# Kernel tuning notes

Measured on AMD Instinct MI355X. Metric: run time of the kernel, lower is better.

Reference implementation:

```python
import math
import jax, jax.numpy as jnp
import numpy as np

NUM_BUCKETS = 32
MAX_DISTANCE = 128
B, T, E, H, D = 2, 2048, 1024, 16, 64
INIT_SCALE = 0.1


def _relative_position_bucket(rel, num_buckets=NUM_BUCKETS, max_distance=MAX_DISTANCE):
    # T5-style bucketing; rel is int [T, T]
    nb = num_buckets // 2
    buckets = (rel > 0).astype(jnp.int32) * nb
    rel_abs = jnp.abs(rel)
    max_exact = nb // 2
    is_small = rel_abs < max_exact
    # guard log(0); those positions are selected by is_small anyway
    val_large = max_exact + (
        jnp.log(jnp.maximum(rel_abs, 1).astype(jnp.float32) / max_exact)
        / math.log(max_distance / max_exact) * (nb - max_exact)
    ).astype(jnp.int32)
    val_large = jnp.minimum(val_large, nb - 1)
    return buckets + jnp.where(is_small, rel_abs, val_large)


def setup_inputs() -> dict:
    key = jax.random.key(0)
    ks = jax.random.split(key, 6)
    x = jax.random.normal(ks[0], (B, T, E), dtype=jnp.float32)
    # nn.Linear weights are [out_features, in_features], init normal(std=0.1)
    Wq = jax.random.normal(ks[1], (H * D, E), dtype=jnp.float32) * INIT_SCALE
    Wk = jax.random.normal(ks[2], (H * D, E), dtype=jnp.float32) * INIT_SCALE
    Wv = jax.random.normal(ks[3], (H * D, E), dtype=jnp.float32) * INIT_SCALE
    Wo = jax.random.normal(ks[4], (E, H * D), dtype=jnp.float32) * INIT_SCALE
    # nn.Embedding default init: standard normal
    rel_emb = jax.random.normal(ks[5], (NUM_BUCKETS, H), dtype=jnp.float32)
    return {"x": x, "Wq": Wq, "Wk": Wk, "Wv": Wv, "Wo": Wo, "rel_emb": rel_emb}


def reference(x, Wq, Wk, Wv, Wo, rel_emb):
    b, t, _ = x.shape
    scale = D ** (-0.5)
    q = jnp.einsum('bte,fe->btf', x, Wq).reshape(b, t, H, D).transpose(0, 2, 1, 3)
    k = jnp.einsum('bte,fe->btf', x, Wk).reshape(b, t, H, D).transpose(0, 2, 1, 3)
    v = jnp.einsum('bte,fe->btf', x, Wv).reshape(b, t, H, D).transpose(0, 2, 1, 3)
    attn = jnp.einsum('bhtd,bhsd->bhts', q, k) * scale  # [B,H,T,T]
    # T5 relative position bias
    pos = jnp.arange(t)
    rel = pos[:, None] - pos[None, :]
    buckets = _relative_position_bucket(rel)
    bias = rel_emb[buckets]                    # [T,T,H]
    attn = attn + bias.transpose(2, 0, 1)[None]  # [1,H,T,T]
    # causal mask (triu, diagonal=1)
    causal = jnp.triu(jnp.ones((t, t), dtype=bool), k=1)
    attn = jnp.where(causal[None, None], -jnp.inf, attn)
    attn = jax.nn.softmax(attn, axis=-1)
    out = jnp.einsum('bhts,bhsd->bhtd', attn, v).transpose(0, 2, 1, 3).reshape(b, t, H * D)
    return jnp.einsum('btf,ef->bte', out, Wo)
```

## Files before the change

kernel.cpp:

```cpp
#include <hip/hip_runtime.h>
#include <hip/hip_bf16.h>
#include <stdint.h>


typedef __attribute__((ext_vector_type(8))) short bf16x8;
typedef __attribute__((ext_vector_type(4))) float f32x4;

#define MFMA16(a, b, c) __builtin_amdgcn_mfma_f32_16x16x32_bf16((a), (b), (c), 0, 0, 0)

typedef __attribute__((address_space(1))) void gvoid_t;
typedef __attribute__((address_space(3))) void lvoid_t;

__device__ __forceinline__ void gload16(const void* g, void* l) {
    __builtin_amdgcn_global_load_lds((gvoid_t*)g, (lvoid_t*)l, 16, 0, 0);
}

__device__ __forceinline__ ushort f2bf_rne(float f) {
    union { float f; uint32_t u; } v; v.f = f;
    uint32_t u = v.u;
    return (ushort)((u + 0x7FFFu + ((u >> 16) & 1u)) >> 16);
}

__global__ void cvt_all(const float* __restrict__ x,
                        const float* __restrict__ wq, const float* __restrict__ wk,
                        const float* __restrict__ wv, const float* __restrict__ wo,
                        ushort* __restrict__ out) {
    int i = (blockIdx.x * 256 + threadIdx.x) * 4;
    int sel = i >> 20;
    const float* src; int off;
    if (sel < 4) { src = x; off = i; }
    else {
        src = (sel == 4) ? wq : (sel == 5) ? wk : (sel == 6) ? wv : wo;
        off = i & 1048575;
    }
    float4 f = *(const float4*)(src + off);
    ushort4 o;
    o.x = f2bf_rne(f.x); o.y = f2bf_rne(f.y);
    o.z = f2bf_rne(f.z); o.w = f2bf_rne(f.w);
    *(ushort4*)(out + i) = o;
}

__global__ void build_bias(const float* __restrict__ rel_emb, float* __restrict__ bias_tab) {
    int idx = blockIdx.x * 256 + threadIdx.x;
    int h = idx >> 11, rel = idx & 2047;
    int bucket;
    if (rel == 0) bucket = 0;
    else if (rel < 8) bucket = 16 + rel;
    else {
        int t;
        if      (rel >= 91) t = 7;
        else if (rel >= 64) t = 6;
        else if (rel >= 46) t = 5;
        else if (rel >= 32) t = 4;
        else if (rel >= 23) t = 3;
        else if (rel >= 16) t = 2;
        else if (rel >= 12) t = 1;
        else                t = 0;
        bucket = 24 + t;
    }
    bias_tab[idx] = rel_emb[bucket * 16 + h];
}

template<int MODE>
__global__ __launch_bounds__(256, MODE == 0 ? 3 : 2) void gemm_bt(
    const ushort* __restrict__ A,
    const ushort* __restrict__ W0, const ushort* __restrict__ W1, const ushort* __restrict__ W2,
    ushort* __restrict__ outq, ushort* __restrict__ outk, ushort* __restrict__ outvt,
    float* __restrict__ outf)
{
    constexpr int BM = (MODE == 0) ? 128 : 64;
    constexpr int AG = BM / 64;
    constexpr int MI = (MODE == 0) ? 4 : 2;
    __shared__ __align__(16) ushort lsA[2][BM * 32];
    __shared__ __align__(16) ushort lsB[2][128 * 32];
    const int tid = threadIdx.x;
    const int lane = tid & 63, w = tid >> 6;
    const int g = lane >> 4, c16 = lane & 15;
    const int wm = w >> 1, wn = w & 1;

    const ushort* W;
    int n0, widx = 0, m0;
    if (MODE == 0) {
        const int bid = blockIdx.x;
        const int xcd = bid & 7, idx = bid >> 3;
        const int yp = xcd * 3 + idx % 3;
        m0 = (idx / 3) * 128;
        widx = yp >> 3;
        W = (widx == 0) ? W0 : (widx == 1) ? W1 : W2;
        n0 = (yp & 7) * 128;
    } else {
        W = W0;
        n0 = blockIdx.y * 128;
        m0 = blockIdx.x * BM;
    }

    f32x4 acc[MI][4];
    #pragma unroll
    for (int i = 0; i < MI; i++)
        #pragma unroll
        for (int j = 0; j < 4; j++) acc[i][j] = (f32x4){0.f, 0.f, 0.f, 0.f};

    int acrow[AG], acj[AG], bcrow[2], bcj[2];
    #pragma unroll
    for (int i = 0; i < AG; i++) {
        int c = (i * 4 + w) * 64 + lane;
        acrow[i] = c >> 2; acj[i] = (c & 3) ^ ((acrow[i] >> 1) & 3);
    }
    #pragma unroll
    for (int i = 0; i < 2; i++) {
        int c = (i * 4 + w) * 64 + lane;
        bcrow[i] = c >> 2; bcj[i] = (c & 3) ^ ((bcrow[i] >> 1) & 3);
    }

    auto stage = [&](int buf, int kt) {
        #pragma unroll
        for (int i = 0; i < AG; i++)
            gload16(A + (size_t)(m0 + acrow[i]) * 1024 + kt + acj[i] * 8,
                    &lsA[buf][(i * 4 + w) * 512]);
        #pragma unroll
        for (int i = 0; i < 2; i++)
            gload16(W + (size_t)(n0 + bcrow[i]) * 1024 + kt + bcj[i] * 8,
                    &lsB[buf][(i * 4 + w) * 512]);
    };

    auto compute = [&](int cur) {
        bf16x8 af[MI], bfv[4];
        #pragma unroll
        for (int mi = 0; mi < MI; mi++) {
            int row = wm * (16 * MI) + mi * 16 + c16;
            af[mi] = *(const bf16x8*)(&lsA[cur][row * 32 + ((g ^ ((row >> 1) & 3)) * 8)]);
        }
        #pragma unroll
        for (int ni = 0; ni < 4; ni++) {
            int row = wn * 64 + ni * 16 + c16;
            bfv[ni] = *(const bf16x8*)(&lsB[cur][row * 32 + ((g ^ ((row >> 1) & 3)) * 8)]);
        }
        #pragma unroll
        for (int mi = 0; mi < MI; mi++)
            #pragma unroll
            for (int ni = 0; ni < 4; ni++)
                acc[mi][ni] = MFMA16(af[mi], bfv[ni], acc[mi][ni]);
    };

    stage(0, 0);
    stage(1, 32);
    for (int t = 0; t < 31; ++t) {
        if constexpr (MODE == 0) asm volatile("s_waitcnt vmcnt(4)" ::: "memory");
        else                     asm volatile("s_waitcnt vmcnt(3)" ::: "memory");
        __builtin_amdgcn_s_barrier();
        const int cur = t & 1;
        compute(cur);
        __builtin_amdgcn_s_barrier();
        if (t < 30) stage(cur, (t + 2) * 32);
    }
    asm volatile("s_waitcnt vmcnt(0)" ::: "memory");
    __builtin_amdgcn_s_barrier();
    compute(1);

    const float qs = (MODE == 0 && widx == 0) ? 0.125f : 1.0f;
    #pragma unroll
    for (int mi = 0; mi < MI; mi++) {
        #pragma unroll
        for (int ni = 0; ni < 4; ni++) {
            int mg = m0 + wm * (16 * MI) + mi * 16 + g * 4;
            if (MODE == 0) {
                int f = n0 + wn * 64 + ni * 16 + c16;
                int h = f >> 6, d = f & 63;
                if (widx < 2) {
                    ushort* dst = (widx == 0) ? outq : outk;
                    #pragma unroll
                    for (int r = 0; r < 4; r++) {
                        int m = mg + r, b = m >> 11, t = m & 2047;
                        dst[((b * 16 + h) * 2048 + t) * 64 + d] = f2bf_rne(acc[mi][ni][r] * qs);
                    }
                } else {
                    int b = mg >> 11, t = mg & 2047;
                    ushort4 pk;
                    pk.x = f2bf_rne(acc[mi][ni][0]); pk.y = f2bf_rne(acc[mi][ni][1]);
                    pk.z = f2bf_rne(acc[mi][ni][2]); pk.w = f2bf_rne(acc[mi][ni][3]);
                    *(ushort4*)(outvt + ((size_t)(b * 16 + h) * 64 + d) * 2048 + t) = pk;
                }
            } else {
                int ng = n0 + wn * 64 + ni * 16 + c16;
                #pragma unroll
                for (int r = 0; r < 4; r++) {
                    int m = mg + r;
                    outf[(size_t)m * 1024 + ng] = acc[mi][ni][r];
                }
            }
        }
    }
}

__global__ __launch_bounds__(256, 4) void attn_kernel(
    const ushort* __restrict__ qb_, const ushort* __restrict__ kb_,
    const ushort* __restrict__ vtb, const float* __restrict__ bias_tab,
    ushort* __restrict__ ob)
{
    __shared__ __align__(16) ushort Ks[64 * 64];
    __shared__ __align__(16) ushort Vs[64 * 64];
    __shared__ __align__(16) ushort Ps[4][16 * 72];

    const int tid = threadIdx.x, lane = tid & 63, w = tid >> 6;
    const int g = lane >> 4, c16 = lane & 15;
    const int p = blockIdx.x;
    const int xcd = p & 7, j = p >> 3;
    const int round = j >> 5, px = j & 31;
    const int bh = (xcd << 2) | round;
    const int qb = (round & 1) ? (31 - px) : px;
    const int b = bh >> 4, h = bh & 15;

    const ushort* qh = qb_ + (size_t)bh * 2048 * 64;
    const ushort* kh = kb_ + (size_t)bh * 2048 * 64;
    const ushort* vh = vtb + (size_t)bh * 64 * 2048;
    const float* bt = bias_tab + h * 2048;
    const float bias_far = bt[128];
    const int q0 = qb * 64;
    const int qrow = q0 + w * 16 + c16;

    int crow[2], cj[2];
    #pragma unroll
    for (int i = 0; i < 2; i++) {
        int c = (i * 4 + w) * 64 + lane;
        crow[i] = c >> 3;
        cj[i] = (c & 7) ^ (crow[i] & 7);
    }

    bf16x8 qf[2];
    #pragma unroll
    for (int kk = 0; kk < 2; kk++)
        qf[kk] = *(const bf16x8*)(qh + (size_t)qrow * 64 + kk * 32 + g * 8);

    float m_run = -1e30f, l_run = 0.f;
    f32x4 o[4];
    #pragma unroll
    for (int ni = 0; ni < 4; ni++) o[ni] = (f32x4){0.f, 0.f, 0.f, 0.f};

    for (int j64 = 0; j64 <= qb; j64++) {
        const int k0 = j64 * 64;
        __syncthreads();
        #pragma unroll
        for (int i = 0; i < 2; i++) {
            gload16(kh + (size_t)(k0 + crow[i]) * 64 + cj[i] * 8, Ks + (i * 4 + w) * 512);
            gload16(vh + (size_t)crow[i] * 2048 + k0 + cj[i] * 8, Vs + (i * 4 + w) * 512);
        }
        __syncthreads();

        f32x4 s[4];
        #pragma unroll
        for (int f = 0; f < 4; f++) s[f] = (f32x4){0.f, 0.f, 0.f, 0.f};
        __builtin_amdgcn_s_setprio(1);
        #pragma unroll
        for (int kk = 0; kk < 2; kk++) {
            #pragma unroll
            for (int f = 0; f < 4; f++) {
                int row = f * 16 + c16;
                bf16x8 a = *(const bf16x8*)(Ks + row * 64 + (((kk * 4 + g) ^ (row & 7)) * 8));
                s[f] = MFMA16(a, qf[kk], s[f]);
            }
        }
        __builtin_amdgcn_s_setprio(0);

        const bool near = (qb - j64) < 3;
        const bool diag = (j64 == qb);
        float p4[4][4];
        float m_new, lt = 0.f;
        if (near) {
            float mt = -1e30f;
            #pragma unroll
            for (int f = 0; f < 4; f++)
                #pragma unroll
                for (int r = 0; r < 4; r++) {
                    int kpos = k0 + f * 16 + g * 4 + r;
                    int rel = qrow - kpos;
                    float lg;
                    if (diag && rel < 0) lg = -1e30f;
                    else lg = s[f][r] + bt[rel];
                    p4[f][r] = lg;
                    mt = fmaxf(mt, lg);
                }
            mt = fmaxf(mt, __shfl_xor(mt, 16));
            mt = fmaxf(mt, __shfl_xor(mt, 32));
            m_new = fmaxf(m_run, mt);
            #pragma unroll
            for (int f = 0; f < 4; f++)
                #pragma unroll
                for (int r = 0; r < 4; r++) {
                    float e = __expf(p4[f][r] - m_new);
                    p4[f][r] = e;
                    lt += e;
                }
        } else {
            float mt = -1e30f;
            #pragma unroll
            for (int f = 0; f < 4; f++)
                #pragma unroll
                for (int r = 0; r < 4; r++) mt = fmaxf(mt, s[f][r]);
            mt = fmaxf(mt, __shfl_xor(mt, 16));
            mt = fmaxf(mt, __shfl_xor(mt, 32));
            m_new = fmaxf(m_run, mt + bias_far);
            float madj = m_new - bias_far;
            #pragma unroll
            for (int f = 0; f < 4; f++)
                #pragma unroll
                for (int r = 0; r < 4; r++) {
                    float e = __expf(s[f][r] - madj);
                    p4[f][r] = e;
                    lt += e;
                }
        }
        lt += __shfl_xor(lt, 16);
        lt += __shfl_xor(lt, 32);
        float alpha = __expf(m_run - m_new);
        l_run = l_run * alpha + lt;
        m_run = m_new;
        #pragma unroll
        for (int ni = 0; ni < 4; ni++) {
            o[ni][0] *= alpha; o[ni][1] *= alpha; o[ni][2] *= alpha; o[ni][3] *= alpha;
        }

        #pragma unroll
        for (int f = 0; f < 4; f++) {
            ushort4 pk;
            pk.x = f2bf_rne(p4[f][0]); pk.y = f2bf_rne(p4[f][1]);
            pk.z = f2bf_rne(p4[f][2]); pk.w = f2bf_rne(p4[f][3]);
            *(ushort4*)(&Ps[w][c16 * 72 + f * 16 + g * 4]) = pk;
        }
        __builtin_amdgcn_s_setprio(1);
        #pragma unroll
        for (int kk = 0; kk < 2; kk++) {
            bf16x8 pf = *(const bf16x8*)(&Ps[w][c16 * 72 + kk * 32 + g * 8]);
            #pragma unroll
            for (int ni = 0; ni < 4; ni++) {
                int row = ni * 16 + c16;
                bf16x8 av = *(const bf16x8*)(Vs + row * 64 + (((kk * 4 + g) ^ (row & 7)) * 8));
                o[ni] = MFMA16(av, pf, o[ni]);
            }
        }
        __builtin_amdgcn_s_setprio(0);
    }

    float inv = 1.f / l_run;
    size_t base = ((size_t)(b * 2048 + qrow)) * 1024 + h * 64;
    #pragma unroll
    for (int ni = 0; ni < 4; ni++) {
        ushort4 pk;
        pk.x = f2bf_rne(o[ni][0] * inv); pk.y = f2bf_rne(o[ni][1] * inv);
        pk.z = f2bf_rne(o[ni][2] * inv); pk.w = f2bf_rne(o[ni][3] * inv);
        *(ushort4*)(ob + base + ni * 16 + g * 4) = pk;
    }
}

extern "C" void kernel_launch(void* const* d_in, const int* in_sizes, int n_in,
                              void* d_out, int out_size, void* d_ws, size_t ws_size,
                              hipStream_t stream) {
    const float* x       = (const float*)d_in[0];
    const float* Wq      = (const float*)d_in[1];
    const float* Wk      = (const float*)d_in[2];
    const float* Wv      = (const float*)d_in[3];
    const float* Wo      = (const float*)d_in[4];
    const float* rel_emb = (const float*)d_in[5];

    char* ws = (char*)d_ws;
    ushort* xbf = (ushort*)(ws);
    ushort* wqb = (ushort*)(ws + (8u  << 20));
    ushort* wkb = (ushort*)(ws + (10u << 20));
    ushort* wvb = (ushort*)(ws + (12u << 20));
    ushort* wob = (ushort*)(ws + (14u << 20));
    ushort* qbf = (ushort*)(ws + (16u << 20));
    ushort* kbf = (ushort*)(ws + (24u << 20));
    ushort* vtb = (ushort*)(ws + (32u << 20));
    ushort* obf = (ushort*)(ws + (40u << 20));
    float*  btab = (float*)(ws + (48u << 20));

    cvt_all<<<8192, 256, 0, stream>>>(x, Wq, Wk, Wv, Wo, xbf);
    build_bias<<<128, 256, 0, stream>>>(rel_emb, btab);

    gemm_bt<0><<<768, 256, 0, stream>>>(xbf, wqb, wkb, wvb, qbf, kbf, vtb, nullptr);
    attn_kernel<<<1024, 256, 0, stream>>>(qbf, kbf, vtb, btab, obf);
    gemm_bt<1><<<dim3(64, 8), 256, 0, stream>>>(obf, wob, nullptr, nullptr,
                                                nullptr, nullptr, nullptr, (float*)d_out);
}
```

Baseline: 185.4 us.

## Widen QKV GEMM tile to 128x256 with 512 threads and fuse prep kernels

The QKV projection GEMM now uses 512-thread blocks with a 128x256 output tile (8 waves, each 64x64) on a plain 2D grid, so each A tile is reused across twice as many output columns. The earlier XCD-aware block swizzle is dropped. The fp32-to-bf16 conversion and the bias-table build are merged into one launch to save a kernel launch. The larger tile increases LDS use per block and halves the number of blocks, which may reduce occupancy and change L2 locality.

```diff
diff --git a/kernel.cpp b/kernel.cpp
--- a/kernel.cpp
+++ b/kernel.cpp
@@ -21,73 +21,76 @@
     return (ushort)((u + 0x7FFFu + ((u >> 16) & 1u)) >> 16);
 }
 
-__global__ void cvt_all(const float* __restrict__ x,
-                        const float* __restrict__ wq, const float* __restrict__ wk,
-                        const float* __restrict__ wv, const float* __restrict__ wo,
-                        ushort* __restrict__ out) {
-    int i = (blockIdx.x * 256 + threadIdx.x) * 4;
-    int sel = i >> 20;
-    const float* src; int off;
-    if (sel < 4) { src = x; off = i; }
-    else {
-        src = (sel == 4) ? wq : (sel == 5) ? wk : (sel == 6) ? wv : wo;
-        off = i & 1048575;
-    }
-    float4 f = *(const float4*)(src + off);
-    ushort4 o;
-    o.x = f2bf_rne(f.x); o.y = f2bf_rne(f.y);
-    o.z = f2bf_rne(f.z); o.w = f2bf_rne(f.w);
-    *(ushort4*)(out + i) = o;
-}
-
-__global__ void build_bias(const float* __restrict__ rel_emb, float* __restrict__ bias_tab) {
-    int idx = blockIdx.x * 256 + threadIdx.x;
-    int h = idx >> 11, rel = idx & 2047;
-    int bucket;
-    if (rel == 0) bucket = 0;
-    else if (rel < 8) bucket = 16 + rel;
-    else {
-        int t;
-        if      (rel >= 91) t = 7;
-        else if (rel >= 64) t = 6;
-        else if (rel >= 46) t = 5;
-        else if (rel >= 32) t = 4;
-        else if (rel >= 23) t = 3;
-        else if (rel >= 16) t = 2;
-        else if (rel >= 12) t = 1;
-        else                t = 0;
-        bucket = 24 + t;
-    }
-    bias_tab[idx] = rel_emb[bucket * 16 + h];
+__global__ void cvt_all_bias(const float* __restrict__ x,
+                             const float* __restrict__ wq, const float* __restrict__ wk,
+                             const float* __restrict__ wv, const float* __restrict__ wo,
+                             const float* __restrict__ rel_emb,
+                             ushort* __restrict__ out, float* __restrict__ bias_tab) {
+    int bid = blockIdx.x;
+    if (bid < 8192) {
+        int i = (bid * 256 + threadIdx.x) * 4;
+        int sel = i >> 20;
+        const float* src; int off;
+        if (sel < 4) { src = x; off = i; }
+        else {
+            src = (sel == 4) ? wq : (sel == 5) ? wk : (sel == 6) ? wv : wo;
+            off = i & 1048575;
+        }
+        float4 f = *(const float4*)(src + off);
+        ushort4 o;
+        o.x = f2bf_rne(f.x); o.y = f2bf_rne(f.y);
+        o.z = f2bf_rne(f.z); o.w = f2bf_rne(f.w);
+        *(ushort4*)(out + i) = o;
+    } else {
+        int idx = (bid - 8192) * 256 + threadIdx.x;
+        int h = idx >> 11, rel = idx & 2047;
+        int bucket;
+        if (rel == 0) bucket = 0;
+        else if (rel < 8) bucket = 16 + rel;
+        else {
+            int t;
+            if      (rel >= 91) t = 7;
+            else if (rel >= 64) t = 6;
+            else if (rel >= 46) t = 5;
+            else if (rel >= 32) t = 4;
+            else if (rel >= 23) t = 3;
+            else if (rel >= 16) t = 2;
+            else if (rel >= 12) t = 1;
+            else                t = 0;
+            bucket = 24 + t;
+        }
+        bias_tab[idx] = rel_emb[bucket * 16 + h];
+    }
 }
 
 template<int MODE>
-__global__ __launch_bounds__(256, MODE == 0 ? 3 : 2) void gemm_bt(
+__global__ __launch_bounds__(MODE == 0 ? 512 : 256, MODE == 0 ? 4 : 2) void gemm_bt(
     const ushort* __restrict__ A,
     const ushort* __restrict__ W0, const ushort* __restrict__ W1, const ushort* __restrict__ W2,
     ushort* __restrict__ outq, ushort* __restrict__ outk, ushort* __restrict__ outvt,
     float* __restrict__ outf)
 {
     constexpr int BM = (MODE == 0) ? 128 : 64;
-    constexpr int AG = BM / 64;
+    constexpr int BN = (MODE == 0) ? 256 : 128;
     constexpr int MI = (MODE == 0) ? 4 : 2;
+    constexpr int ALOADS = (MODE == 0) ? 1 : 1;
+    constexpr int BLOADS = 2;
     __shared__ __align__(16) ushort lsA[2][BM * 32];
-    __shared__ __align__(16) ushort lsB[2][128 * 32];
+    __shared__ __align__(16) ushort lsB[2][BN * 32];
     const int tid = threadIdx.x;
     const int lane = tid & 63, w = tid >> 6;
     const int g = lane >> 4, c16 = lane & 15;
-    const int wm = w >> 1, wn = w & 1;
+    const int wrow = (MODE == 0) ? (w >> 2) * 64 : (w >> 1) * 32;
+    const int wcol = (MODE == 0) ? (w & 3) * 64 : (w & 1) * 64;
 
     const ushort* W;
     int n0, widx = 0, m0;
     if (MODE == 0) {
-        const int bid = blockIdx.x;
-        const int xcd = bid & 7, idx = bid >> 3;
-        const int yp = xcd * 3 + idx % 3;
-        m0 = (idx / 3) * 128;
-        widx = yp >> 3;
+        m0 = blockIdx.x * BM;
+        const int yp = blockIdx.y;
+        widx = yp >> 2;
         W = (widx == 0) ? W0 : (widx == 1) ? W1 : W2;
-        n0 = (yp & 7) * 128;
+        n0 = (yp & 3) * 256;
     } else {
         W = W0;
         n0 = blockIdx.y * 128;
@@ -100,39 +103,40 @@
         #pragma unroll
         for (int j = 0; j < 4; j++) acc[i][j] = (f32x4){0.f, 0.f, 0.f, 0.f};
 
-    int acrow[AG], acj[AG], bcrow[2], bcj[2];
-    #pragma unroll
-    for (int i = 0; i < AG; i++) {
-        int c = (i * 4 + w) * 64 + lane;
+    int acrow[ALOADS], acj[ALOADS], bcrow[BLOADS], bcj[BLOADS];
+    constexpr int NT = (MODE == 0) ? 512 : 256;
+    #pragma unroll
+    for (int i = 0; i < ALOADS; i++) {
+        int c = i * NT + tid;
         acrow[i] = c >> 2; acj[i] = (c & 3) ^ ((acrow[i] >> 1) & 3);
     }
     #pragma unroll
-    for (int i = 0; i < 2; i++) {
-        int c = (i * 4 + w) * 64 + lane;
+    for (int i = 0; i < BLOADS; i++) {
+        int c = i * NT + tid;
         bcrow[i] = c >> 2; bcj[i] = (c & 3) ^ ((bcrow[i] >> 1) & 3);
     }
 
     auto stage = [&](int buf, int kt) {
         #pragma unroll
-        for (int i = 0; i < AG; i++)
+        for (int i = 0; i < ALOADS; i++)
             gload16(A + (size_t)(m0 + acrow[i]) * 1024 + kt + acj[i] * 8,
-                    &lsA[buf][(i * 4 + w) * 512]);
-        #pragma unroll
-        for (int i = 0; i < 2; i++)
+                    &lsA[buf][(i * (NT / 64) + w) * 512]);
+        #pragma unroll
+        for (int i = 0; i < BLOADS; i++)
             gload16(W + (size_t)(n0 + bcrow[i]) * 1024 + kt + bcj[i] * 8,
-                    &lsB[buf][(i * 4 + w) * 512]);
+                    &lsB[buf][(i * (NT / 64) + w) * 512]);
     };
 
     auto compute = [&](int cur) {
         bf16x8 af[MI], bfv[4];
         #pragma unroll
         for (int mi = 0; mi < MI; mi++) {
-            int row = wm * (16 * MI) + mi * 16 + c16;
+            int row = wrow + mi * 16 + c16;
             af[mi] = *(const bf16x8*)(&lsA[cur][row * 32 + ((g ^ ((row >> 1) & 3)) * 8)]);
         }
         #pragma unroll
         for (int ni = 0; ni < 4; ni++) {
-            int row = wn * 64 + ni * 16 + c16;
+            int row = wcol + ni * 16 + c16;
             bfv[ni] = *(const bf16x8*)(&lsB[cur][row * 32 + ((g ^ ((row >> 1) & 3)) * 8)]);
         }
         #pragma unroll
@@ -145,8 +149,7 @@
     stage(0, 0);
     stage(1, 32);
     for (int t = 0; t < 31; ++t) {
-        if constexpr (MODE == 0) asm volatile("s_waitcnt vmcnt(4)" ::: "memory");
-        else                     asm volatile("s_waitcnt vmcnt(3)" ::: "memory");
+        asm volatile("s_waitcnt vmcnt(3)" ::: "memory");
         __builtin_amdgcn_s_barrier();
         const int cur = t & 1;
         compute(cur);
@@ -162,9 +165,9 @@
     for (int mi = 0; mi < MI; mi++) {
         #pragma unroll
         for (int ni = 0; ni < 4; ni++) {
-            int mg = m0 + wm * (16 * MI) + mi * 16 + g * 4;
+            int mg = m0 + wrow + mi * 16 + g * 4;
             if (MODE == 0) {
-                int f = n0 + wn * 64 + ni * 16 + c16;
+                int f = n0 + wcol + ni * 16 + c16;
                 int h = f >> 6, d = f & 63;
                 if (widx < 2) {
                     ushort* dst = (widx == 0) ? outq : outk;
@@ -181,7 +184,7 @@
                     *(ushort4*)(outvt + ((size_t)(b * 16 + h) * 64 + d) * 2048 + t) = pk;
                 }
             } else {
-                int ng = n0 + wn * 64 + ni * 16 + c16;
+                int ng = n0 + wcol + ni * 16 + c16;
                 #pragma unroll
                 for (int r = 0; r < 4; r++) {
                     int m = mg + r;
@@ -373,10 +376,9 @@
     ushort* obf = (ushort*)(ws + (40u << 20));
     float*  btab = (float*)(ws + (48u << 20));
 
-    cvt_all<<<8192, 256, 0, stream>>>(x, Wq, Wk, Wv, Wo, xbf);
-    build_bias<<<128, 256, 0, stream>>>(rel_emb, btab);
-
-    gemm_bt<0><<<768, 256, 0, stream>>>(xbf, wqb, wkb, wvb, qbf, kbf, vtb, nullptr);
+    cvt_all_bias<<<8320, 256, 0, stream>>>(x, Wq, Wk, Wv, Wo, rel_emb, xbf, btab);
+
+    gemm_bt<0><<<dim3(32, 12), 512, 0, stream>>>(xbf, wqb, wkb, wvb, qbf, kbf, vtb, nullptr);
     attn_kernel<<<1024, 256, 0, stream>>>(qbf, kbf, vtb, btab, obf);
     gemm_bt<1><<<dim3(64, 8), 256, 0, stream>>>(obf, wob, nullptr, nullptr,
                                                 nullptr, nullptr, nullptr, (float*)d_out);
```

After: 182.2 us. No clear change (-1.7%).
